# Performance work log

Measured on AMD Instinct MI355X. Metric: run time of the kernel, lower is better.

## Reference

```python
import jax, jax.numpy as jnp
import numpy as np

V, D, N, K = 500000, 64, 50000, 32


def setup_inputs() -> dict:
    key = jax.random.key(0)
    ks = jax.random.split(key, 8)
    return {
        "embeddings": jax.random.normal(ks[0], (V, D), dtype=jnp.float32),
        "W1": jax.random.normal(ks[1], (2 * D, D), dtype=jnp.float32) * 0.05,
        "b1": jnp.zeros((D,), dtype=jnp.float32),
        "W2": jax.random.normal(ks[2], (D, D), dtype=jnp.float32) * 0.05,
        "b2": jnp.zeros((D,), dtype=jnp.float32),
        "w3": jax.random.normal(ks[3], (D, 1), dtype=jnp.float32) * 0.05,
        "b3": jnp.zeros((1,), dtype=jnp.float32),
        "video_nodes": jax.random.randint(ks[4], (N,), 0, V, dtype=jnp.int32),
        "neigh_idx": jax.random.randint(ks[5], (N, K), 0, V, dtype=jnp.int32),
        "neigh_deg": jax.random.randint(ks[6], (N,), 0, K + 1, dtype=jnp.int32),
    }


def reference(embeddings, W1, b1, W2, b2, w3, b3, video_nodes, neigh_idx, neigh_deg):
    # Ragged neighbor gather (padded to K, masked by degree)
    e = embeddings[neigh_idx]                      # [N, K, D] neighbor embeddings
    u = embeddings[video_nodes]                    # [N, D]    center embeddings
    # GraphRec-style attention: MLP on [neigh, center] concat -> scalar score
    x = jnp.concatenate(
        [e, jnp.broadcast_to(u[:, None, :], e.shape)], axis=-1)  # [N, K, 2D]
    h = jax.nn.relu(x @ W1 + b1)
    h = jax.nn.relu(h @ W2 + b2)
    s = (h @ w3)[..., 0] + b3[0]                   # [N, K]
    mask = jnp.arange(K)[None, :] < neigh_deg[:, None]
    s = jnp.where(mask, s, -1e9)                   # mask padded neighbors
    att = jax.nn.softmax(s, axis=-1)               # softmax over valid neighbors
    out = jnp.einsum('nkd,nk->nd', e, att)         # attention-weighted sum
    # num_neighs == 0 -> fall back to node's own embedding
    out = jnp.where((neigh_deg > 0)[:, None], out, u)
    return out
```

## Files before the change

kernel.cpp:

```cpp
#include <hip/hip_runtime.h>
#include <hip/hip_bf16.h>

typedef __bf16 bf16x8 __attribute__((ext_vector_type(8)));
typedef float  f32x4  __attribute__((ext_vector_type(4)));

#define MFMA32(acc, a, b) acc = __builtin_amdgcn_mfma_f32_16x16x32_bf16(a, b, acc, 0, 0, 0)
#define LD4(p) (*(const float4*)(p))

__device__ __forceinline__ bf16x8 cvt8(float4 a, float4 b) {
  bf16x8 r;
  r[0] = (__bf16)a.x; r[1] = (__bf16)a.y; r[2] = (__bf16)a.z; r[3] = (__bf16)a.w;
  r[4] = (__bf16)b.x; r[5] = (__bf16)b.y; r[6] = (__bf16)b.z; r[7] = (__bf16)b.w;
  return r;
}

template <int CTRL>
__device__ __forceinline__ float dpp_mov(float x) {
  int yi = __builtin_amdgcn_update_dpp(0, __builtin_bit_cast(int, x), CTRL, 0xF, 0xF, true);
  return __builtin_bit_cast(float, yi);
}
template <int CTRL>
__device__ __forceinline__ float dpp_fadd(float x) { return x + dpp_mov<CTRL>(x); }

__device__ __forceinline__ float tree16(const float* o, int lr) {
  float q8[8];
#pragma unroll
  for (int t = 0; t < 8; t++) {
    const bool up = (lr & 8);
    float sel = up ? o[t + 8] : o[t];
    float oth = up ? o[t] : o[t + 8];
    q8[t] = sel + dpp_mov<0x128>(oth);
  }
  float q4[4];
#pragma unroll
  for (int t = 0; t < 4; t++) {
    const bool up = (lr & 4);
    float sel = up ? q8[t + 4] : q8[t];
    float oth = up ? q8[t] : q8[t + 4];
    q4[t] = sel + __shfl_xor(oth, 4);
  }
  float q2[2];
#pragma unroll
  for (int t = 0; t < 2; t++) {
    const bool up = (lr & 2);
    float sel = up ? q4[t + 2] : q4[t];
    float oth = up ? q4[t] : q4[t + 2];
    q2[t] = sel + dpp_mov<0x4E>(oth);
  }
  const bool up = (lr & 1);
  float sel = up ? q2[1] : q2[0];
  float oth = up ? q2[0] : q2[1];
  return sel + dpp_mov<0xB1>(oth);
}

__global__ void prep_frags(const float* __restrict__ W1,
                           const float* __restrict__ W2,
                           __bf16* __restrict__ wf) {
  int idx = blockIdx.x * 256 + threadIdx.x;
  if (idx < 8192) {
    int j = idx & 7, lane = (idx >> 3) & 63, mt = (idx >> 9) & 3, ks = idx >> 11;
    int i = ks * 32 + ((lane >> 4) << 3) + j;
    int col = mt * 16 + (lane & 15);
    wf[idx] = (__bf16)W1[i * 64 + col];
  } else if (idx < 12288) {
    int t = idx - 8192;
    int j = t & 7, lane = (t >> 3) & 63, mt2 = (t >> 9) & 3, ks2 = (t >> 11) & 1;
    int g = (lane >> 4) & 3;
    int rho = (ks2 * 2 + (j >> 2)) * 16 + g * 4 + (j & 3);
    wf[idx] = (__bf16)W2[rho * 64 + mt2 * 16 + (lane & 15)];
  }
}

__global__ __launch_bounds__(512) void graph_agg(
    const float* __restrict__ emb,
    const float* __restrict__ b1g, const float* __restrict__ b2g,
    const float* __restrict__ w3g,
    const int* __restrict__ vn, const int* __restrict__ ni,
    const int* __restrict__ nd,
    const __bf16* __restrict__ wf,
    float* __restrict__ out, int N) {
  __shared__ __align__(16) unsigned char smem[25344];

  {
    const uint4* src = (const uint4*)wf;
    uint4* dst = (uint4*)smem;
#pragma unroll
    for (int i = 0; i < 3; i++) dst[threadIdx.x + i * 512] = src[threadIdx.x + i * 512];
    int t = threadIdx.x;
    if (t < 64) {
      ((float*)(smem + 24576))[t] = b1g[t];
      ((float*)(smem + 24832))[t] = b2g[t];
      ((float*)(smem + 25088))[t] = w3g[t];
    }
  }
  __syncthreads();

  const __bf16* w1f = (const __bf16*)smem;
  const __bf16* w2f = (const __bf16*)(smem + 16384);
  const int wid = threadIdx.x >> 6;
  const int l   = threadIdx.x & 63;
  const int g   = l >> 4;
  const int lr  = l & 15;

  const int gw = blockIdx.x * 8 + wid;
  const int nwaves = gridDim.x * 8;

  int n = gw;
  int node = 0, deg = 0, i0 = 0, i1 = 0;
  if (n < N) {
    node = vn[n]; deg = nd[n];
    i0 = ni[(long)n * 32 + lr]; i1 = ni[(long)n * 32 + 16 + lr];
  }

  for (; n < N; n += nwaves) {
    const int cn = node, cd = deg, ci0 = i0, ci1 = i1;
    {
      int nn = n + nwaves; if (nn >= N) nn = n;
      node = vn[nn]; deg = nd[nn];
      i0 = ni[(long)nn * 32 + lr]; i1 = ni[(long)nn * 32 + 16 + lr];
    }
    const float* ub = emb + (long)cn * 64;

    if (cd == 0) {
      out[(long)n * 64 + l] = ub[l];
      continue;
    }
    const bool m1 = (cd > 16);

    int boff = 24576;
    asm volatile("" : "+v"(boff));
    const unsigned char* bb = smem + boff;

    bf16x8 ef00, ef01, ef10, ef11;
    {
      const int a = (lr < cd) ? ci0 : cn;
      const float* p = emb + (long)a * 64 + g * 8;
      ef00 = cvt8(LD4(p), LD4(p + 4));
      ef01 = cvt8(LD4(p + 32), LD4(p + 36));
    }
    if (m1) {
      const int a = (16 + lr < cd) ? ci1 : cn;
      const float* p = emb + (long)a * 64 + g * 8;
      ef10 = cvt8(LD4(p), LD4(p + 4));
      ef11 = cvt8(LD4(p + 32), LD4(p + 36));
    }
    bf16x8 uf0, uf1;
    {
      const float* q = ub + g * 8;
      uf0 = cvt8(LD4(q), LD4(q + 4));
      uf1 = cvt8(LD4(q + 32), LD4(q + 36));
    }

    f32x4 acc[4][2];
#pragma unroll
    for (int mt = 0; mt < 4; mt++) {
      f32x4 bv = *(const f32x4*)(bb + (mt * 16 + g * 4) * 4);
      acc[mt][0] = bv; acc[mt][1] = bv;
    }
    const bf16x8 xb0s[4] = {ef00, ef01, uf0, uf1};
    const bf16x8 xb1s[4] = {ef10, ef11, uf0, uf1};
#pragma unroll
    for (int ks = 0; ks < 4; ks++) {
#pragma unroll
      for (int mt = 0; mt < 4; mt++) {
        bf16x8 wa = *(const bf16x8*)(w1f + ((ks * 4 + mt) * 64 + l) * 8);
        MFMA32(acc[mt][0], wa, xb0s[ks]);
        if (m1) MFMA32(acc[mt][1], wa, xb1s[ks]);
      }
    }

    bf16x8 hb[2][2];
#pragma unroll
    for (int ks2 = 0; ks2 < 2; ks2++)
#pragma unroll
      for (int nt = 0; nt < 2; nt++) {
        if (nt == 0 || m1) {
          bf16x8 v;
#pragma unroll
          for (int j = 0; j < 8; j++) {
            const int mt = ks2 * 2 + (j >> 2), r = j & 3;
            v[j] = (__bf16)fmaxf(acc[mt][nt][r], 0.f);
          }
          hb[ks2][nt] = v;
        }
      }

#pragma unroll
    for (int mt2 = 0; mt2 < 4; mt2++) {
      f32x4 bv = *(const f32x4*)(bb + 256 + (mt2 * 16 + g * 4) * 4);
      acc[mt2][0] = bv; acc[mt2][1] = bv;
    }
#pragma unroll
    for (int ks2 = 0; ks2 < 2; ks2++)
#pragma unroll
      for (int mt2 = 0; mt2 < 4; mt2++) {
        bf16x8 wa = *(const bf16x8*)(w2f + ((ks2 * 4 + mt2) * 64 + l) * 8);
        MFMA32(acc[mt2][0], wa, hb[ks2][0]);
        if (m1) MFMA32(acc[mt2][1], wa, hb[ks2][1]);
      }

    float sv0 = 0.f, sv1 = 0.f;
#pragma unroll
    for (int mt2 = 0; mt2 < 4; mt2++) {
      f32x4 wv = *(const f32x4*)(bb + 512 + (mt2 * 16 + g * 4) * 4);
#pragma unroll
      for (int r = 0; r < 4; r++) {
        sv0 += fmaxf(acc[mt2][0][r], 0.f) * wv[r];
        if (m1) sv1 += fmaxf(acc[mt2][1][r], 0.f) * wv[r];
      }
    }
    sv0 += __shfl_xor(sv0, 16); sv0 += __shfl_xor(sv0, 32);
    if (m1) { sv1 += __shfl_xor(sv1, 16); sv1 += __shfl_xor(sv1, 32); }

    const bool v0 = (lr < cd);
    const bool v1 = m1 && (16 + lr < cd);
    float p0 = v0 ? __expf(sv0) : 0.f;
    float p1 = v1 ? __expf(sv1) : 0.f;
    float sum = p0 + p1;
    sum = dpp_fadd<0x128>(sum);
    sum = dpp_fadd<0x124>(sum);
    sum = dpp_fadd<0x122>(sum);
    sum = dpp_fadd<0x121>(sum);
    const float inv = 1.f / sum;
    const float a0 = p0 * inv, a1 = p1 * inv;

    float o[16];
#pragma unroll
    for (int j = 0; j < 8; j++) {
      float v = a0 * (float)ef00[j];
      if (m1) v += a1 * (float)ef10[j];
      o[j] = v;
      float w = a0 * (float)ef01[j];
      if (m1) w += a1 * (float)ef11[j];
      o[8 + j] = w;
    }
    const int dim = ((lr >> 3) << 5) + g * 8 + (lr & 7);
    out[(long)n * 64 + dim] = tree16(o, lr);
  }
}

extern "C" void kernel_launch(void* const* d_in, const int* in_sizes, int n_in,
                              void* d_out, int out_size, void* d_ws, size_t ws_size,
                              hipStream_t stream) {
  const float* emb = (const float*)d_in[0];
  const float* W1  = (const float*)d_in[1];
  const float* b1  = (const float*)d_in[2];
  const float* W2  = (const float*)d_in[3];
  const float* b2  = (const float*)d_in[4];
  const float* w3  = (const float*)d_in[5];
  const int* vn = (const int*)d_in[7];
  const int* ni = (const int*)d_in[8];
  const int* nd = (const int*)d_in[9];
  float* out = (float*)d_out;
  const int N = in_sizes[7];
  __bf16* wf = (__bf16*)d_ws;

  prep_frags<<<48, 256, 0, stream>>>(W1, W2, wf);
  graph_agg<<<2048, 512, 0, stream>>>(emb, b1, b2, w3, vn, ni, nd, wf, out, N);
}
```

Baseline: 74.42 us.

## Split aggregation into light and heavy kernels by neighbor degree

Replaces the single aggregation kernel with two kernels. One handles nodes with degree ≤16 using a single 16-neighbor MFMA tile, and the other handles degree >16 with two tiles and no per-node branches. This aims to remove the divergent m1 branching and the register pressure of carrying both tiles for light nodes. In exchange it adds a second launch, and both kernels scan every node's metadata and reload the weights into shared memory.

```diff
diff --git a/kernel.cpp b/kernel.cpp
--- a/kernel.cpp
+++ b/kernel.cpp
@@ -71,7 +71,7 @@
   }
 }
 
-__global__ __launch_bounds__(512) void graph_agg(
+__global__ __launch_bounds__(512) void agg_light(
     const float* __restrict__ emb,
     const float* __restrict__ b1g, const float* __restrict__ b2g,
     const float* __restrict__ w3g,
@@ -80,7 +80,6 @@
     const __bf16* __restrict__ wf,
     float* __restrict__ out, int N) {
   __shared__ __align__(16) unsigned char smem[25344];
-
   {
     const uint4* src = (const uint4*)wf;
     uint4* dst = (uint4*)smem;
@@ -106,10 +105,148 @@
   const int nwaves = gridDim.x * 8;
 
   int n = gw;
+  int node = 0, deg = 0, i0 = 0;
+  if (n < N) {
+    node = vn[n]; deg = nd[n];
+    i0 = (deg <= 16) ? ni[(long)n * 32 + lr] : 0;
+  }
+
+  for (; n < N; n += nwaves) {
+    const int cn = node, cd = deg, ci0 = i0;
+    {
+      int nn = n + nwaves; if (nn >= N) nn = n;
+      node = vn[nn]; deg = nd[nn];
+      i0 = (deg <= 16) ? ni[(long)nn * 32 + lr] : 0;
+    }
+    if (cd > 16) continue;
+
+    const float* ub = emb + (long)cn * 64;
+    if (cd == 0) {
+      out[(long)n * 64 + l] = ub[l];
+      continue;
+    }
+
+    int boff = 24576;
+    asm volatile("" : "+v"(boff));
+    const unsigned char* bb = smem + boff;
+
+    bf16x8 ef0, ef1, uf0, uf1;
+    {
+      const int a = (lr < cd) ? ci0 : cn;
+      const float* p = emb + (long)a * 64 + g * 8;
+      ef0 = cvt8(LD4(p), LD4(p + 4));
+      ef1 = cvt8(LD4(p + 32), LD4(p + 36));
+      const float* q = ub + g * 8;
+      uf0 = cvt8(LD4(q), LD4(q + 4));
+      uf1 = cvt8(LD4(q + 32), LD4(q + 36));
+    }
+
+    f32x4 acc[4];
+#pragma unroll
+    for (int mt = 0; mt < 4; mt++)
+      acc[mt] = *(const f32x4*)(bb + (mt * 16 + g * 4) * 4);
+    const bf16x8 xs[4] = {ef0, ef1, uf0, uf1};
+#pragma unroll
+    for (int ks = 0; ks < 4; ks++)
+#pragma unroll
+      for (int mt = 0; mt < 4; mt++) {
+        bf16x8 wa = *(const bf16x8*)(w1f + ((ks * 4 + mt) * 64 + l) * 8);
+        MFMA32(acc[mt], wa, xs[ks]);
+      }
+
+    bf16x8 hb[2];
+#pragma unroll
+    for (int ks2 = 0; ks2 < 2; ks2++) {
+      bf16x8 v;
+#pragma unroll
+      for (int j = 0; j < 8; j++) {
+        const int mt = ks2 * 2 + (j >> 2), r = j & 3;
+        v[j] = (__bf16)fmaxf(acc[mt][r], 0.f);
+      }
+      hb[ks2] = v;
+    }
+
+#pragma unroll
+    for (int mt2 = 0; mt2 < 4; mt2++)
+      acc[mt2] = *(const f32x4*)(bb + 256 + (mt2 * 16 + g * 4) * 4);
+#pragma unroll
+    for (int ks2 = 0; ks2 < 2; ks2++)
+#pragma unroll
+      for (int mt2 = 0; mt2 < 4; mt2++) {
+        bf16x8 wa = *(const bf16x8*)(w2f + ((ks2 * 4 + mt2) * 64 + l) * 8);
+        MFMA32(acc[mt2], wa, hb[ks2]);
+      }
+
+    float sv = 0.f;
+#pragma unroll
+    for (int mt2 = 0; mt2 < 4; mt2++) {
+      f32x4 wv = *(const f32x4*)(bb + 512 + (mt2 * 16 + g * 4) * 4);
+#pragma unroll
+      for (int r = 0; r < 4; r++)
+        sv += fmaxf(acc[mt2][r], 0.f) * wv[r];
+    }
+    sv += __shfl_xor(sv, 16);
+    sv += __shfl_xor(sv, 32);
+
+    const float p0 = (lr < cd) ? __expf(sv) : 0.f;
+    float sum = p0;
+    sum = dpp_fadd<0x128>(sum);
+    sum = dpp_fadd<0x124>(sum);
+    sum = dpp_fadd<0x122>(sum);
+    sum = dpp_fadd<0x121>(sum);
+    const float a0 = p0 / sum;
+
+    float o[16];
+#pragma unroll
+    for (int j = 0; j < 8; j++) {
+      o[j]     = a0 * (float)ef0[j];
+      o[8 + j] = a0 * (float)ef1[j];
+    }
+    const int dim = ((lr >> 3) << 5) + g * 8 + (lr & 7);
+    out[(long)n * 64 + dim] = tree16(o, lr);
+  }
+}
+
+__global__ __launch_bounds__(512) void agg_heavy(
+    const float* __restrict__ emb,
+    const float* __restrict__ b1g, const float* __restrict__ b2g,
+    const float* __restrict__ w3g,
+    const int* __restrict__ vn, const int* __restrict__ ni,
+    const int* __restrict__ nd,
+    const __bf16* __restrict__ wf,
+    float* __restrict__ out, int N) {
+  __shared__ __align__(16) unsigned char smem[25344];
+  {
+    const uint4* src = (const uint4*)wf;
+    uint4* dst = (uint4*)smem;
+#pragma unroll
+    for (int i = 0; i < 3; i++) dst[threadIdx.x + i * 512] = src[threadIdx.x + i * 512];
+    int t = threadIdx.x;
+    if (t < 64) {
+      ((float*)(smem + 24576))[t] = b1g[t];
+      ((float*)(smem + 24832))[t] = b2g[t];
+      ((float*)(smem + 25088))[t] = w3g[t];
+    }
+  }
+  __syncthreads();
+
+  const __bf16* w1f = (const __bf16*)smem;
+  const __bf16* w2f = (const __bf16*)(smem + 16384);
+  const int wid = threadIdx.x >> 6;
+  const int l   = threadIdx.x & 63;
+  const int g   = l >> 4;
+  const int lr  = l & 15;
+
+  const int gw = blockIdx.x * 8 + wid;
+  const int nwaves = gridDim.x * 8;
+
+  int n = gw;
   int node = 0, deg = 0, i0 = 0, i1 = 0;
   if (n < N) {
     node = vn[n]; deg = nd[n];
-    i0 = ni[(long)n * 32 + lr]; i1 = ni[(long)n * 32 + 16 + lr];
+    const bool h = (deg > 16);
+    i0 = h ? ni[(long)n * 32 + lr] : 0;
+    i1 = h ? ni[(long)n * 32 + 16 + lr] : 0;
   }
 
   for (; n < N; n += nwaves) {
@@ -117,34 +254,30 @@
     {
       int nn = n + nwaves; if (nn >= N) nn = n;
       node = vn[nn]; deg = nd[nn];
-      i0 = ni[(long)nn * 32 + lr]; i1 = ni[(long)nn * 32 + 16 + lr];
-    }
+      const bool h = (deg > 16);
+      i0 = h ? ni[(long)nn * 32 + lr] : 0;
+      i1 = h ? ni[(long)nn * 32 + 16 + lr] : 0;
+    }
+    if (cd <= 16) continue;
+
     const float* ub = emb + (long)cn * 64;
-
-    if (cd == 0) {
-      out[(long)n * 64 + l] = ub[l];
-      continue;
-    }
-    const bool m1 = (cd > 16);
 
     int boff = 24576;
     asm volatile("" : "+v"(boff));
     const unsigned char* bb = smem + boff;
 
-    bf16x8 ef00, ef01, ef10, ef11;
-    {
-      const int a = (lr < cd) ? ci0 : cn;
-      const float* p = emb + (long)a * 64 + g * 8;
+    bf16x8 ef00, ef01, ef10, ef11, uf0, uf1;
+    {
+      const float* p = emb + (long)ci0 * 64 + g * 8;
       ef00 = cvt8(LD4(p), LD4(p + 4));
       ef01 = cvt8(LD4(p + 32), LD4(p + 36));
     }
-    if (m1) {
+    {
       const int a = (16 + lr < cd) ? ci1 : cn;
       const float* p = emb + (long)a * 64 + g * 8;
       ef10 = cvt8(LD4(p), LD4(p + 4));
       ef11 = cvt8(LD4(p + 32), LD4(p + 36));
     }
-    bf16x8 uf0, uf1;
     {
       const float* q = ub + g * 8;
       uf0 = cvt8(LD4(q), LD4(q + 4));
@@ -160,29 +293,26 @@
     const bf16x8 xb0s[4] = {ef00, ef01, uf0, uf1};
     const bf16x8 xb1s[4] = {ef10, ef11, uf0, uf1};
 #pragma unroll
-    for (int ks = 0; ks < 4; ks++) {
+    for (int ks = 0; ks < 4; ks++)
 #pragma unroll
       for (int mt = 0; mt < 4; mt++) {
         bf16x8 wa = *(const bf16x8*)(w1f + ((ks * 4 + mt) * 64 + l) * 8);
         MFMA32(acc[mt][0], wa, xb0s[ks]);
-        if (m1) MFMA32(acc[mt][1], wa, xb1s[ks]);
-      }
-    }
+        MFMA32(acc[mt][1], wa, xb1s[ks]);
+      }
 
     bf16x8 hb[2][2];
 #pragma unroll
     for (int ks2 = 0; ks2 < 2; ks2++)
 #pragma unroll
       for (int nt = 0; nt < 2; nt++) {
-        if (nt == 0 || m1) {
-          bf16x8 v;
-#pragma unroll
-          for (int j = 0; j < 8; j++) {
-            const int mt = ks2 * 2 + (j >> 2), r = j & 3;
-            v[j] = (__bf16)fmaxf(acc[mt][nt][r], 0.f);
-          }
-          hb[ks2][nt] = v;
+        bf16x8 v;
+#pragma unroll
+        for (int j = 0; j < 8; j++) {
+          const int mt = ks2 * 2 + (j >> 2), r = j & 3;
+          v[j] = (__bf16)fmaxf(acc[mt][nt][r], 0.f);
         }
+        hb[ks2][nt] = v;
       }
 
 #pragma unroll
@@ -196,7 +326,7 @@
       for (int mt2 = 0; mt2 < 4; mt2++) {
         bf16x8 wa = *(const bf16x8*)(w2f + ((ks2 * 4 + mt2) * 64 + l) * 8);
         MFMA32(acc[mt2][0], wa, hb[ks2][0]);
-        if (m1) MFMA32(acc[mt2][1], wa, hb[ks2][1]);
+        MFMA32(acc[mt2][1], wa, hb[ks2][1]);
       }
 
     float sv0 = 0.f, sv1 = 0.f;
@@ -206,16 +336,15 @@
 #pragma unroll
       for (int r = 0; r < 4; r++) {
         sv0 += fmaxf(acc[mt2][0][r], 0.f) * wv[r];
-        if (m1) sv1 += fmaxf(acc[mt2][1][r], 0.f) * wv[r];
+        sv1 += fmaxf(acc[mt2][1][r], 0.f) * wv[r];
       }
     }
     sv0 += __shfl_xor(sv0, 16); sv0 += __shfl_xor(sv0, 32);
-    if (m1) { sv1 += __shfl_xor(sv1, 16); sv1 += __shfl_xor(sv1, 32); }
-
-    const bool v0 = (lr < cd);
-    const bool v1 = m1 && (16 + lr < cd);
-    float p0 = v0 ? __expf(sv0) : 0.f;
-    float p1 = v1 ? __expf(sv1) : 0.f;
+    sv1 += __shfl_xor(sv1, 16); sv1 += __shfl_xor(sv1, 32);
+
+    const bool v1 = (16 + lr < cd);
+    const float p0 = __expf(sv0);
+    const float p1 = v1 ? __expf(sv1) : 0.f;
     float sum = p0 + p1;
     sum = dpp_fadd<0x128>(sum);
     sum = dpp_fadd<0x124>(sum);
@@ -227,12 +356,8 @@
     float o[16];
 #pragma unroll
     for (int j = 0; j < 8; j++) {
-      float v = a0 * (float)ef00[j];
-      if (m1) v += a1 * (float)ef10[j];
-      o[j] = v;
-      float w = a0 * (float)ef01[j];
-      if (m1) w += a1 * (float)ef11[j];
-      o[8 + j] = w;
+      o[j]     = a0 * (float)ef00[j] + a1 * (float)ef10[j];
+      o[8 + j] = a0 * (float)ef01[j] + a1 * (float)ef11[j];
     }
     const int dim = ((lr >> 3) << 5) + g * 8 + (lr & 7);
     out[(long)n * 64 + dim] = tree16(o, lr);
@@ -256,5 +381,6 @@
   __bf16* wf = (__bf16*)d_ws;
 
   prep_frags<<<48, 256, 0, stream>>>(W1, W2, wf);
-  graph_agg<<<2048, 512, 0, stream>>>(emb, b1, b2, w3, vn, ni, nd, wf, out, N);
-}
+  agg_light<<<2048, 512, 0, stream>>>(emb, b1, b2, w3, vn, ni, nd, wf, out, N);
+  agg_heavy<<<2048, 512, 0, stream>>>(emb, b1, b2, w3, vn, ni, nd, wf, out, N);
+}
```

Result: slower. 99.90 us (+34.2%).
